# Performance work log

Hardware: AMD Instinct MI355X
Metric: run time of the kernel (lower is better)

The kernel has to match this reference:

```python
import jax, jax.numpy as jnp
import numpy as np

B, S = 1024, 512
V, E, H, T = 50000, 300, 800, 50


def setup_inputs() -> dict:
    key = jax.random.key(0)
    ks = jax.random.split(key, 8)
    ids = jax.random.randint(ks[0], (B, S), 0, V, dtype=jnp.int64 if jax.config.jax_enable_x64 else jnp.int32)
    return {
        "ids": ids,
        "rho": jax.random.normal(ks[1], (V, E), jnp.float32) * 0.02,
        "alpha": jax.random.normal(ks[2], (T, E), jnp.float32) * 0.02,
        "W1": jax.random.normal(ks[3], (E, H), jnp.float32) * 0.05,
        "b1": jnp.zeros((H,), jnp.float32),
        "Wmu": jax.random.normal(ks[4], (H, T), jnp.float32) * 0.05,
        "bmu": jnp.zeros((T,), jnp.float32),
        "Wlv": jax.random.normal(ks[5], (H, T), jnp.float32) * 0.05,
        "blv": jnp.zeros((T,), jnp.float32),
    }


def reference(ids, rho, alpha, W1, b1, Wmu, bmu, Wlv, blv):
    b, s = ids.shape
    v = rho.shape[0]
    # bag-of-words histogram: scatter-add instead of dense one_hot+reduce_sum
    bows = jnp.zeros((b, v), rho.dtype).at[jnp.arange(b)[:, None], ids].add(1.0)
    # zero out special tokens 1 and 2 (original: x * (1 - sum(one_hot([1,2]))))
    bows = bows.at[:, jnp.array([1, 2])].set(0.0)
    normal_bows = bows / jnp.sum(bows, axis=-1, keepdims=True)
    # encoder (eval mode: dropout is identity)
    x = jnp.einsum('bv,ve->be', normal_bows, rho)
    h = jax.nn.relu(x @ W1 + b1)
    mu_theta = h @ Wmu + bmu
    logsigma_theta = h @ Wlv + blv
    kl_theta = -0.5 * jnp.sum(1.0 + logsigma_theta - mu_theta**2 - jnp.exp(logsigma_theta), axis=-1)
    # reparameterize (eval/inference mode): z = mu
    theta = jax.nn.softmax(mu_theta, axis=-1)  # [B, T]
    beta = jax.nn.softmax(jnp.einsum('te,ve->tv', alpha, rho), axis=-1)  # [T, V]
    lookup = jnp.log(theta @ beta + 1e-5)  # [B, V]
    recon_loss = -jnp.sum(lookup * bows, axis=-1)
    loss = jnp.mean(recon_loss) + jnp.mean(kl_theta)
    return theta, loss
```

## Files before the change

kernel.cpp:

```cpp
#include <hip/hip_runtime.h>
#include <math.h>


#define Bn 1024
#define Sn 512
#define Vn 50000
#define En 300
#define Hn 800
#define Tn 50
#define KP 320
#define BSTR 64
#define W1FRAG_N (50 * 10 * 64 * 8)
#define WFRAG_N  (8 * 25 * 64 * 8)
#define NRANGE 8
#define VRANGE (Vn / NRANGE)

typedef __bf16 bf16x8 __attribute__((ext_vector_type(8)));
typedef float  f32x4  __attribute__((ext_vector_type(4)));

__device__ __forceinline__ float waveReduceSum(float v) {
    #pragma unroll
    for (int off = 32; off > 0; off >>= 1) v += __shfl_xor(v, off, 64);
    return v;
}
__device__ __forceinline__ float waveReduceMax(float v) {
    #pragma unroll
    for (int off = 32; off > 0; off >>= 1) v = fmaxf(v, __shfl_xor(v, off, 64));
    return v;
}
__device__ __forceinline__ unsigned short f2bf(float x) {
    unsigned u = __float_as_uint(x);
    return (unsigned short)((u + 0x7FFFu + ((u >> 16) & 1u)) >> 16);
}
__device__ __forceinline__ float bf_lo(unsigned u) { return __uint_as_float(u << 16); }
__device__ __forceinline__ float bf_hi(unsigned u) { return __uint_as_float(u & 0xFFFF0000u); }

__global__ __launch_bounds__(256) void k0_init(
        const float* __restrict__ alpha, unsigned short* __restrict__ bfrag,
        float* __restrict__ topicsum, float* __restrict__ loss,
        float* __restrict__ xbar) {
    const int gid = blockIdx.x * 256 + threadIdx.x;
    if (blockIdx.x == 0) {
        if (threadIdx.x < Tn) topicsum[threadIdx.x] = 0.f;
        if (threadIdx.x == 63) *loss = 0.f;
    }
    if (gid < Bn * En) xbar[gid] = 0.f;
    if (gid < 4 * 10 * 64 * 8) {
        int j = gid & 7;
        int lane = (gid >> 3) & 63;
        int rest = gid >> 9;
        int kt = rest % 10, w = rest / 10;
        int t = 16 * w + (lane & 15);
        int e = kt * 32 + (lane >> 4) * 8 + j;
        bfrag[gid] = (t < Tn && e < En) ? f2bf(alpha[t * En + e]) : (unsigned short)0;
    }
}

__global__ __launch_bounds__(256) void kp_prep(
        const float* __restrict__ W1, const float* __restrict__ Wmu,
        const float* __restrict__ Wlv, unsigned short* __restrict__ w1frag,
        unsigned short* __restrict__ wfrag) {
    const int gid = blockIdx.x * 256 + threadIdx.x;
    if (gid < W1FRAG_N) {
        int j = gid & 7, lane = (gid >> 3) & 63, rest = gid >> 9;
        int kt = rest % 10, nt = rest / 10;
        int e = kt * 32 + (lane >> 4) * 8 + j;
        int hcol = nt * 16 + (lane & 15);
        w1frag[gid] = (e < En) ? f2bf(W1[e * Hn + hcol]) : (unsigned short)0;
    } else {
        int g2 = gid - W1FRAG_N;
        if (g2 < WFRAG_N) {
            int j = g2 & 7, lane = (g2 >> 3) & 63, rest = g2 >> 9;
            int kt = rest % 25, nt = rest / 25;
            int k = kt * 32 + (lane >> 4) * 8 + j;
            int t = (nt & 3) * 16 + (lane & 15);
            float val = 0.f;
            if (t < Tn) val = (nt < 4) ? Wmu[k * Tn + t] : Wlv[k * Tn + t];
            wfrag[g2] = f2bf(val);
        }
    }
}

__global__ __launch_bounds__(256) void k5_cast(
        const float4* __restrict__ rho4, ushort4* __restrict__ rhoh4) {
    const int i = blockIdx.x * 256 + threadIdx.x;
    if (i < Vn * (KP / 4)) {
        int v = i / (KP / 4), s = i - v * (KP / 4);
        ushort4 p = {0, 0, 0, 0};
        if (s < En / 4) {
            float4 r = rho4[v * (En / 4) + s];
            p.x = f2bf(r.x); p.y = f2bf(r.y); p.z = f2bf(r.z); p.w = f2bf(r.w);
        }
        rhoh4[i] = p;
    }
}

__global__ __launch_bounds__(256) void k4_beta(
        const unsigned short* __restrict__ rhoh,
        const unsigned short* __restrict__ bfrag,
        unsigned int* __restrict__ betaU32, float* __restrict__ topicsum) {
    __shared__ unsigned short trans[64 * 66];
    const int tid = threadIdx.x;
    const int wave = tid >> 6, lane = tid & 63;
    const int quad = lane >> 4, l15 = lane & 15;
    const int v0 = blockIdx.x * 64;

    bf16x8 bf[10];
    #pragma unroll
    for (int kt = 0; kt < 10; ++kt)
        bf[kt] = *(const bf16x8*)(bfrag + ((wave * 10 + kt) * 64 + lane) * 8);

    float ts = 0.f;
    #pragma unroll
    for (int mt = 0; mt < 4; ++mt) {
        const int vbase = v0 + mt * 16;
        int vrow = vbase + l15; if (vrow >= Vn) vrow = Vn - 1;
        const unsigned short* arow = rhoh + (size_t)vrow * KP + quad * 8;
        f32x4 acc = {0.f, 0.f, 0.f, 0.f};
        #pragma unroll
        for (int kt = 0; kt < 10; ++kt) {
            bf16x8 a = *(const bf16x8*)(arow + kt * 32);
            acc = __builtin_amdgcn_mfma_f32_16x16x32_bf16(a, bf[kt], acc, 0, 0, 0);
        }
        #pragma unroll
        for (int r = 0; r < 4; ++r) {
            int vv = vbase + quad * 4 + r;
            float ev = (vv < Vn) ? expf(acc[r]) : 0.f;
            ts += ev;
            trans[(mt * 16 + quad * 4 + r) * 66 + 16 * wave + l15] = f2bf(ev);
        }
    }
    ts += __shfl_xor(ts, 16, 64);
    ts += __shfl_xor(ts, 32, 64);
    const int t = 16 * wave + l15;
    if (lane < 16 && t < Tn) atomicAdd(&topicsum[t], ts);
    __syncthreads();
    unsigned int* dst = betaU32 + (size_t)v0 * 32;
    const unsigned int* tr32 = (const unsigned int*)trans;
    for (int i = tid; i < 64 * 32; i += 256)
        dst[i] = tr32[(i >> 5) * 33 + (i & 31)];
}

__global__ __launch_bounds__(256) void k1_tokens_x(
        const int* __restrict__ ids, const unsigned int* __restrict__ rhoh32,
        int* __restrict__ toks, int* __restrict__ cnt,
        float* __restrict__ xbar) {
    __shared__ int sid[Sn];
    __shared__ int sfid[Sn];
    __shared__ int scount, sfull;
    const int blk = blockIdx.x;
    const int r = blk & (NRANGE - 1), b = blk >> 3;
    const int tid = threadIdx.x;
    const int lo = r * VRANGE, hi = lo + VRANGE;
    if (tid == 0) { scount = 0; sfull = 0; }
    __syncthreads();
    #pragma unroll
    for (int s0 = 0; s0 < Sn; s0 += 256) {
        int id = ids[b * Sn + s0 + tid];
        bool val = (id != 1 && id != 2);
        if (val && id >= lo && id < hi) {
            int p = atomicAdd(&scount, 1);
            sid[p] = id;
        }
        if (r == 0 && val) {
            int p = atomicAdd(&sfull, 1);
            sfid[p] = id;
        }
    }
    __syncthreads();
    if (r == 0) {
        const int nf = sfull;
        for (int i = tid; i < nf; i += 256) toks[b * Sn + i] = sfid[i];
        if (tid == 0) cnt[b] = nf;
    }
    const int m = scount;
    if (tid < En / 2) {
        float ax = 0.f, ay = 0.f;
        for (int s = 0; s < m; ++s) {
            unsigned u = rhoh32[sid[s] * (KP / 2) + tid];
            ax += bf_lo(u);
            ay += bf_hi(u);
        }
        if (m > 0) {
            atomicAdd(&xbar[b * En + 2 * tid], ax);
            atomicAdd(&xbar[b * En + 2 * tid + 1], ay);
        }
    }
}

__global__ __launch_bounds__(256) void k2a_xcast(
        const float* __restrict__ xbar, const int* __restrict__ cnt,
        unsigned short* __restrict__ xbh) {
    const int gid = blockIdx.x * 256 + threadIdx.x;
    if (gid < Bn * KP) {
        int b = gid / KP, e = gid - b * KP;
        unsigned short out = 0;
        if (e < En) {
            float invn = 1.0f / (float)cnt[b];
            out = f2bf(xbar[b * En + e] * invn);
        }
        xbh[gid] = out;
    }
}

__global__ __launch_bounds__(256) void k2_h(
        const unsigned short* __restrict__ xbh,
        const unsigned short* __restrict__ w1frag,
        const float* __restrict__ b1, unsigned short* __restrict__ hbh) {
    const int tid = threadIdx.x;
    const int wave = tid >> 6, lane = tid & 63;
    const int quad = lane >> 4, l15 = lane & 15;
    const int b0 = blockIdx.x * 16;
    const int nt = blockIdx.y * 4 + wave;
    if (nt >= 50) return;
    const unsigned short* arow = xbh + (size_t)(b0 + l15) * KP + quad * 8;
    f32x4 acc = {0.f, 0.f, 0.f, 0.f};
    #pragma unroll
    for (int kt = 0; kt < 10; ++kt) {
        bf16x8 a = *(const bf16x8*)(arow + kt * 32);
        bf16x8 bv = *(const bf16x8*)(w1frag + ((size_t)(nt * 10 + kt) * 64 + lane) * 8);
        acc = __builtin_amdgcn_mfma_f32_16x16x32_bf16(a, bv, acc, 0, 0, 0);
    }
    const int col = nt * 16 + l15;
    const float bias = b1[col];
    #pragma unroll
    for (int r = 0; r < 4; ++r) {
        int row = b0 + quad * 4 + r;
        hbh[(size_t)row * Hn + col] = f2bf(fmaxf(acc[r] + bias, 0.f));
    }
}

__global__ __launch_bounds__(256) void k3_theta(
        const unsigned short* __restrict__ hbh,
        const unsigned short* __restrict__ wfrag,
        const float* __restrict__ bmu, const float* __restrict__ blv,
        float* __restrict__ theta, float* __restrict__ loss) {
    __shared__ float mlds[16 * 65];
    __shared__ float llds[16 * 65];
    const int tid = threadIdx.x;
    const int wave = tid >> 6, lane = tid & 63;
    const int quad = lane >> 4, l15 = lane & 15;
    const int b0 = blockIdx.x * 16;
    const unsigned short* arow = hbh + (size_t)(b0 + l15) * Hn + quad * 8;
    f32x4 am = {0.f, 0.f, 0.f, 0.f}, al = {0.f, 0.f, 0.f, 0.f};
    #pragma unroll
    for (int kt = 0; kt < 25; ++kt) {
        bf16x8 a  = *(const bf16x8*)(arow + kt * 32);
        bf16x8 bm = *(const bf16x8*)(wfrag + ((size_t)(wave * 25 + kt) * 64 + lane) * 8);
        bf16x8 bl = *(const bf16x8*)(wfrag + ((size_t)((4 + wave) * 25 + kt) * 64 + lane) * 8);
        am = __builtin_amdgcn_mfma_f32_16x16x32_bf16(a, bm, am, 0, 0, 0);
        al = __builtin_amdgcn_mfma_f32_16x16x32_bf16(a, bl, al, 0, 0, 0);
    }
    const int t = wave * 16 + l15;
    const float bm_ = (t < Tn) ? bmu[t] : 0.f;
    const float bl_ = (t < Tn) ? blv[t] : 0.f;
    #pragma unroll
    for (int r = 0; r < 4; ++r) {
        int row = quad * 4 + r;
        mlds[row * 65 + t] = am[r] + bm_;
        llds[row * 65 + t] = al[r] + bl_;
    }
    __syncthreads();
    const int tt = (lane < Tn) ? lane : (Tn - 1);
    const bool act = (lane < Tn);
    float klacc = 0.f;
    #pragma unroll
    for (int k = 0; k < 4; ++k) {
        int row = wave * 4 + k;
        float mu = mlds[row * 65 + tt];
        float lv = llds[row * 65 + tt];
        float m = waveReduceMax(act ? mu : -1e30f);
        float ex = act ? expf(mu - m) : 0.f;
        float ssum = waveReduceSum(ex);
        if (act) theta[(b0 + row) * Tn + lane] = ex / ssum;
        klacc += waveReduceSum(act ? (1.f + lv - mu * mu - expf(lv)) : 0.f);
    }
    if (lane == 0) atomicAdd(loss, -0.5f * klacc * (1.0f / (float)Bn));
}

__global__ __launch_bounds__(256) void k6_recon(
        const int* __restrict__ toks, const int* __restrict__ cnt,
        const float* __restrict__ theta, const float* __restrict__ topicsum,
        const unsigned short* __restrict__ betaUh, float* __restrict__ loss) {
    __shared__ float sw[Tn];
    __shared__ float swred[4];
    const int b = blockIdx.x, tid = threadIdx.x;
    if (tid < Tn) sw[tid] = theta[b * Tn + tid] / topicsum[tid];
    __syncthreads();
    float wr[Tn];
    #pragma unroll
    for (int t = 0; t < Tn; ++t) wr[t] = sw[t];
    float lsum = 0.f;
    const int n = cnt[b];
    for (int i = tid; i < n; i += 256) {
        int v = toks[b * Sn + i];
        const uint4* q = (const uint4*)(betaUh + (size_t)v * BSTR);
        float dot = 0.f;
        #pragma unroll
        for (int k = 0; k < 6; ++k) {
            uint4 u = q[k];
            int t = 8 * k;
            dot += wr[t]     * bf_lo(u.x) + wr[t + 1] * bf_hi(u.x);
            dot += wr[t + 2] * bf_lo(u.y) + wr[t + 3] * bf_hi(u.y);
            dot += wr[t + 4] * bf_lo(u.z) + wr[t + 5] * bf_hi(u.z);
            dot += wr[t + 6] * bf_lo(u.w) + wr[t + 7] * bf_hi(u.w);
        }
        unsigned d = ((const unsigned*)q)[24];
        dot += wr[48] * bf_lo(d) + wr[49] * bf_hi(d);
        lsum += logf(dot + 1e-5f);
    }
    float s = waveReduceSum(lsum);
    const int wave = tid >> 6, lane = tid & 63;
    if (lane == 0) swred[wave] = s;
    __syncthreads();
    if (tid == 0) {
        float tot = swred[0] + swred[1] + swred[2] + swred[3];
        atomicAdd(loss, -tot * (1.0f / (float)Bn));
    }
}

extern "C" void kernel_launch(void* const* d_in, const int* in_sizes, int n_in,
                              void* d_out, int out_size, void* d_ws, size_t ws_size,
                              hipStream_t stream) {
    const int*   ids   = (const int*)d_in[0];
    const float* rho   = (const float*)d_in[1];
    const float* alpha = (const float*)d_in[2];
    const float* W1    = (const float*)d_in[3];
    const float* b1    = (const float*)d_in[4];
    const float* Wmu   = (const float*)d_in[5];
    const float* bmu   = (const float*)d_in[6];
    const float* Wlv   = (const float*)d_in[7];
    const float* blv   = (const float*)d_in[8];

    float* theta = (float*)d_out;
    float* loss  = theta + Bn * Tn;

    const int k4grid = (Vn + 63) / 64;
    char* w = (char*)d_ws;
    float* topicsum = (float*)w;                w += 256;
    unsigned short* bfrag = (unsigned short*)w; w += 4 * 10 * 64 * 8 * 2;
    unsigned short* w1frag = (unsigned short*)w; w += (size_t)W1FRAG_N * 2;
    unsigned short* wfrag = (unsigned short*)w;  w += (size_t)WFRAG_N * 2;
    int*   cnt      = (int*)w;                  w += Bn * 4;
    int*   toks     = (int*)w;                  w += Bn * Sn * 4;
    float* xbar     = (float*)w;                w += Bn * En * 4;
    unsigned short* xbh = (unsigned short*)w;   w += (size_t)Bn * KP * 2;
    unsigned short* hbh = (unsigned short*)w;   w += (size_t)Bn * Hn * 2;
    unsigned short* rhoh = (unsigned short*)w;  w += (size_t)Vn * KP * 2;
    unsigned int* betaU32 = (unsigned int*)w;   w += (size_t)k4grid * 64 * 128;

    k0_init<<<(Bn * En + 255) / 256, 256, 0, stream>>>(alpha, bfrag, topicsum, loss, xbar);
    kp_prep<<<(W1FRAG_N + WFRAG_N + 255) / 256, 256, 0, stream>>>(
        W1, Wmu, Wlv, w1frag, wfrag);
    k5_cast<<<(Vn * (KP / 4) + 255) / 256, 256, 0, stream>>>(
        (const float4*)rho, (ushort4*)rhoh);
    k4_beta<<<k4grid, 256, 0, stream>>>(rhoh, bfrag, betaU32, topicsum);
    k1_tokens_x<<<Bn * NRANGE, 256, 0, stream>>>(ids, (const unsigned int*)rhoh,
                                                 toks, cnt, xbar);
    k2a_xcast<<<(Bn * KP + 255) / 256, 256, 0, stream>>>(xbar, cnt, xbh);
    k2_h<<<dim3(64, 13), 256, 0, stream>>>(xbh, w1frag, b1, hbh);
    k3_theta<<<64, 256, 0, stream>>>(hbh, wfrag, bmu, blv, theta, loss);
    k6_recon<<<Bn, 256, 0, stream>>>(toks, cnt, theta, topicsum,
                                     (const unsigned short*)betaU32, loss);
}
```

Baseline: 224.3 us.

## Fuse rho bf16 cast into beta kernel and split recon by vocab range

Removes the separate rho cast kernel; the beta kernel now reads fp32 rho, converts it to bf16 in registers, feeds the MFMA and writes the bf16 copy for later use. The token compaction buffer is dropped. The recon kernel now rescans ids per block and splits each batch row across 16 vocabulary ranges to get more parallelism, and the x-gather kernel uses 16 ranges too. This trades an extra ids rescan and more atomics on the loss for fewer launches and less global traffic.

```diff
diff --git a/kernel.cpp b/kernel.cpp
--- a/kernel.cpp
+++ b/kernel.cpp
@@ -12,11 +12,12 @@
 #define BSTR 64
 #define W1FRAG_N (50 * 10 * 64 * 8)
 #define WFRAG_N  (8 * 25 * 64 * 8)
-#define NRANGE 8
+#define NRANGE 16
 #define VRANGE (Vn / NRANGE)
 
 typedef __bf16 bf16x8 __attribute__((ext_vector_type(8)));
 typedef float  f32x4  __attribute__((ext_vector_type(4)));
+typedef unsigned short us8 __attribute__((ext_vector_type(8)));
 
 __device__ __forceinline__ float waveReduceSum(float v) {
     #pragma unroll
@@ -81,24 +82,10 @@
     }
 }
 
-__global__ __launch_bounds__(256) void k5_cast(
-        const float4* __restrict__ rho4, ushort4* __restrict__ rhoh4) {
-    const int i = blockIdx.x * 256 + threadIdx.x;
-    if (i < Vn * (KP / 4)) {
-        int v = i / (KP / 4), s = i - v * (KP / 4);
-        ushort4 p = {0, 0, 0, 0};
-        if (s < En / 4) {
-            float4 r = rho4[v * (En / 4) + s];
-            p.x = f2bf(r.x); p.y = f2bf(r.y); p.z = f2bf(r.z); p.w = f2bf(r.w);
-        }
-        rhoh4[i] = p;
-    }
-}
-
 __global__ __launch_bounds__(256) void k4_beta(
-        const unsigned short* __restrict__ rhoh,
-        const unsigned short* __restrict__ bfrag,
-        unsigned int* __restrict__ betaU32, float* __restrict__ topicsum) {
+        const float* __restrict__ rho, const unsigned short* __restrict__ bfrag,
+        unsigned int* __restrict__ betaU32, unsigned short* __restrict__ rhoh,
+        float* __restrict__ topicsum) {
     __shared__ unsigned short trans[64 * 66];
     const int tid = threadIdx.x;
     const int wave = tid >> 6, lane = tid & 63;
@@ -115,11 +102,28 @@
     for (int mt = 0; mt < 4; ++mt) {
         const int vbase = v0 + mt * 16;
         int vrow = vbase + l15; if (vrow >= Vn) vrow = Vn - 1;
-        const unsigned short* arow = rhoh + (size_t)vrow * KP + quad * 8;
+        const float* arow = rho + (size_t)vrow * En;
+        unsigned short* hrow = rhoh + (size_t)vrow * KP;
         f32x4 acc = {0.f, 0.f, 0.f, 0.f};
         #pragma unroll
         for (int kt = 0; kt < 10; ++kt) {
-            bf16x8 a = *(const bf16x8*)(arow + kt * 32);
+            const int c0 = quad * 8 + kt * 32;
+            float f[8];
+            if (kt < 9) {
+                float4 p = *(const float4*)(arow + c0);
+                float4 q = *(const float4*)(arow + c0 + 4);
+                f[0] = p.x; f[1] = p.y; f[2] = p.z; f[3] = p.w;
+                f[4] = q.x; f[5] = q.y; f[6] = q.z; f[7] = q.w;
+            } else {
+                #pragma unroll
+                for (int i = 0; i < 8; ++i)
+                    f[i] = (c0 + i < En) ? arow[c0 + i] : 0.f;
+            }
+            us8 pk;
+            #pragma unroll
+            for (int i = 0; i < 8; ++i) pk[i] = f2bf(f[i]);
+            *(us8*)(hrow + c0) = pk;
+            bf16x8 a = __builtin_bit_cast(bf16x8, pk);
             acc = __builtin_amdgcn_mfma_f32_16x16x32_bf16(a, bf[kt], acc, 0, 0, 0);
         }
         #pragma unroll
@@ -143,13 +147,11 @@
 
 __global__ __launch_bounds__(256) void k1_tokens_x(
         const int* __restrict__ ids, const unsigned int* __restrict__ rhoh32,
-        int* __restrict__ toks, int* __restrict__ cnt,
-        float* __restrict__ xbar) {
+        int* __restrict__ cnt, float* __restrict__ xbar) {
     __shared__ int sid[Sn];
-    __shared__ int sfid[Sn];
     __shared__ int scount, sfull;
     const int blk = blockIdx.x;
-    const int r = blk & (NRANGE - 1), b = blk >> 3;
+    const int r = blk & (NRANGE - 1), b = blk >> 4;
     const int tid = threadIdx.x;
     const int lo = r * VRANGE, hi = lo + VRANGE;
     if (tid == 0) { scount = 0; sfull = 0; }
@@ -162,29 +164,20 @@
             int p = atomicAdd(&scount, 1);
             sid[p] = id;
         }
-        if (r == 0 && val) {
-            int p = atomicAdd(&sfull, 1);
-            sfid[p] = id;
-        }
-    }
-    __syncthreads();
-    if (r == 0) {
-        const int nf = sfull;
-        for (int i = tid; i < nf; i += 256) toks[b * Sn + i] = sfid[i];
-        if (tid == 0) cnt[b] = nf;
-    }
+        if (r == 0 && val) atomicAdd(&sfull, 1);
+    }
+    __syncthreads();
+    if (r == 0 && tid == 0) cnt[b] = sfull;
     const int m = scount;
-    if (tid < En / 2) {
+    if (tid < En / 2 && m > 0) {
         float ax = 0.f, ay = 0.f;
         for (int s = 0; s < m; ++s) {
             unsigned u = rhoh32[sid[s] * (KP / 2) + tid];
             ax += bf_lo(u);
             ay += bf_hi(u);
         }
-        if (m > 0) {
-            atomicAdd(&xbar[b * En + 2 * tid], ax);
-            atomicAdd(&xbar[b * En + 2 * tid + 1], ay);
-        }
+        atomicAdd(&xbar[b * En + 2 * tid], ax);
+        atomicAdd(&xbar[b * En + 2 * tid + 1], ay);
     }
 }
 
@@ -279,21 +272,36 @@
 }
 
 __global__ __launch_bounds__(256) void k6_recon(
-        const int* __restrict__ toks, const int* __restrict__ cnt,
-        const float* __restrict__ theta, const float* __restrict__ topicsum,
+        const int* __restrict__ ids, const float* __restrict__ theta,
+        const float* __restrict__ topicsum,
         const unsigned short* __restrict__ betaUh, float* __restrict__ loss) {
     __shared__ float sw[Tn];
+    __shared__ int sid[Sn];
+    __shared__ int scount;
     __shared__ float swred[4];
-    const int b = blockIdx.x, tid = threadIdx.x;
+    const int blk = blockIdx.x;
+    const int r = blk & (NRANGE - 1), b = blk >> 4;
+    const int tid = threadIdx.x;
+    const int lo = r * VRANGE, hi = lo + VRANGE;
     if (tid < Tn) sw[tid] = theta[b * Tn + tid] / topicsum[tid];
+    if (tid == 0) scount = 0;
+    __syncthreads();
+    #pragma unroll
+    for (int s0 = 0; s0 < Sn; s0 += 256) {
+        int id = ids[b * Sn + s0 + tid];
+        if (id != 1 && id != 2 && id >= lo && id < hi) {
+            int p = atomicAdd(&scount, 1);
+            sid[p] = id;
+        }
+    }
     __syncthreads();
     float wr[Tn];
     #pragma unroll
     for (int t = 0; t < Tn; ++t) wr[t] = sw[t];
     float lsum = 0.f;
-    const int n = cnt[b];
+    const int n = scount;
     for (int i = tid; i < n; i += 256) {
-        int v = toks[b * Sn + i];
+        int v = sid[i];
         const uint4* q = (const uint4*)(betaUh + (size_t)v * BSTR);
         float dot = 0.f;
         #pragma unroll
@@ -315,7 +323,7 @@
     __syncthreads();
     if (tid == 0) {
         float tot = swred[0] + swred[1] + swred[2] + swred[3];
-        atomicAdd(loss, -tot * (1.0f / (float)Bn));
+        if (tot != 0.f) atomicAdd(loss, -tot * (1.0f / (float)Bn));
     }
 }
 
@@ -342,7 +350,6 @@
     unsigned short* w1frag = (unsigned short*)w; w += (size_t)W1FRAG_N * 2;
     unsigned short* wfrag = (unsigned short*)w;  w += (size_t)WFRAG_N * 2;
     int*   cnt      = (int*)w;                  w += Bn * 4;
-    int*   toks     = (int*)w;                  w += Bn * Sn * 4;
     float* xbar     = (float*)w;                w += Bn * En * 4;
     unsigned short* xbh = (unsigned short*)w;   w += (size_t)Bn * KP * 2;
     unsigned short* hbh = (unsigned short*)w;   w += (size_t)Bn * Hn * 2;
@@ -352,14 +359,12 @@
     k0_init<<<(Bn * En + 255) / 256, 256, 0, stream>>>(alpha, bfrag, topicsum, loss, xbar);
     kp_prep<<<(W1FRAG_N + WFRAG_N + 255) / 256, 256, 0, stream>>>(
         W1, Wmu, Wlv, w1frag, wfrag);
-    k5_cast<<<(Vn * (KP / 4) + 255) / 256, 256, 0, stream>>>(
-        (const float4*)rho, (ushort4*)rhoh);
-    k4_beta<<<k4grid, 256, 0, stream>>>(rhoh, bfrag, betaU32, topicsum);
+    k4_beta<<<k4grid, 256, 0, stream>>>(rho, bfrag, betaU32, rhoh, topicsum);
     k1_tokens_x<<<Bn * NRANGE, 256, 0, stream>>>(ids, (const unsigned int*)rhoh,
-                                                 toks, cnt, xbar);
+                                                 cnt, xbar);
     k2a_xcast<<<(Bn * KP + 255) / 256, 256, 0, stream>>>(xbar, cnt, xbh);
     k2_h<<<dim3(64, 13), 256, 0, stream>>>(xbh, w1frag, b1, hbh);
     k3_theta<<<64, 256, 0, stream>>>(hbh, wfrag, bmu, blv, theta, loss);
-    k6_recon<<<Bn, 256, 0, stream>>>(toks, cnt, theta, topicsum,
-                                     (const unsigned short*)betaU32, loss);
-}
+    k6_recon<<<Bn * NRANGE, 256, 0, stream>>>(ids, theta, topicsum,
+                                              (const unsigned short*)betaU32, loss);
+}
```

Result: slower. 433.2 us (+93.1%).

## Shrink beta tiles to 16 rows, replicate topic sums, merge prep kernels

Applied to the files above, without the earlier changes.

k4_beta now handles 16 vocabulary rows per block instead of 64, so the grid grows from about 782 to 3125 blocks. B fragments are loaded inside the k-loop rather than kept in registers, which lowers register pressure. Topic-sum atomics go to 8 replicated slots, and k6 adds those slots back together, to reduce contention on 50 addresses. The kp_prep weight-fragment kernel is folded into k0_init to save one launch. In exchange, each block does more loads of alpha fragments per row computed, and the final transpose store is done in smaller chunks.

```diff
diff --git a/kernel.cpp b/kernel.cpp
--- a/kernel.cpp
+++ b/kernel.cpp
@@ -36,14 +36,14 @@
 __device__ __forceinline__ float bf_hi(unsigned u) { return __uint_as_float(u & 0xFFFF0000u); }
 
 __global__ __launch_bounds__(256) void k0_init(
-        const float* __restrict__ alpha, unsigned short* __restrict__ bfrag,
-        float* __restrict__ topicsum, float* __restrict__ loss,
-        float* __restrict__ xbar) {
+        const float* __restrict__ alpha, const float* __restrict__ W1,
+        const float* __restrict__ Wmu, const float* __restrict__ Wlv,
+        unsigned short* __restrict__ bfrag, unsigned short* __restrict__ w1frag,
+        unsigned short* __restrict__ wfrag, float* __restrict__ topicsumR,
+        float* __restrict__ loss, float* __restrict__ xbar) {
     const int gid = blockIdx.x * 256 + threadIdx.x;
-    if (blockIdx.x == 0) {
-        if (threadIdx.x < Tn) topicsum[threadIdx.x] = 0.f;
-        if (threadIdx.x == 63) *loss = 0.f;
-    }
+    if (gid < 512) topicsumR[gid] = 0.f;
+    if (gid == 520) *loss = 0.f;
     if (gid < Bn * En) xbar[gid] = 0.f;
     if (gid < 4 * 10 * 64 * 8) {
         int j = gid & 7;
@@ -54,13 +54,6 @@
         int e = kt * 32 + (lane >> 4) * 8 + j;
         bfrag[gid] = (t < Tn && e < En) ? f2bf(alpha[t * En + e]) : (unsigned short)0;
     }
-}
-
-__global__ __launch_bounds__(256) void kp_prep(
-        const float* __restrict__ W1, const float* __restrict__ Wmu,
-        const float* __restrict__ Wlv, unsigned short* __restrict__ w1frag,
-        unsigned short* __restrict__ wfrag) {
-    const int gid = blockIdx.x * 256 + threadIdx.x;
     if (gid < W1FRAG_N) {
         int j = gid & 7, lane = (gid >> 3) & 63, rest = gid >> 9;
         int kt = rest % 10, nt = rest / 10;
@@ -98,46 +91,37 @@
 __global__ __launch_bounds__(256) void k4_beta(
         const unsigned short* __restrict__ rhoh,
         const unsigned short* __restrict__ bfrag,
-        unsigned int* __restrict__ betaU32, float* __restrict__ topicsum) {
-    __shared__ unsigned short trans[64 * 66];
+        unsigned int* __restrict__ betaU32, float* __restrict__ topicsumR) {
+    __shared__ unsigned short trans[16 * 66];
     const int tid = threadIdx.x;
     const int wave = tid >> 6, lane = tid & 63;
     const int quad = lane >> 4, l15 = lane & 15;
-    const int v0 = blockIdx.x * 64;
-
-    bf16x8 bf[10];
-    #pragma unroll
-    for (int kt = 0; kt < 10; ++kt)
-        bf[kt] = *(const bf16x8*)(bfrag + ((wave * 10 + kt) * 64 + lane) * 8);
-
+    const int v0 = blockIdx.x * 16;
+
+    const unsigned short* arow = rhoh + (size_t)(v0 + l15) * KP + quad * 8;
+    f32x4 acc = {0.f, 0.f, 0.f, 0.f};
+    #pragma unroll
+    for (int kt = 0; kt < 10; ++kt) {
+        bf16x8 a = *(const bf16x8*)(arow + kt * 32);
+        bf16x8 bv = *(const bf16x8*)(bfrag + ((wave * 10 + kt) * 64 + lane) * 8);
+        acc = __builtin_amdgcn_mfma_f32_16x16x32_bf16(a, bv, acc, 0, 0, 0);
+    }
     float ts = 0.f;
     #pragma unroll
-    for (int mt = 0; mt < 4; ++mt) {
-        const int vbase = v0 + mt * 16;
-        int vrow = vbase + l15; if (vrow >= Vn) vrow = Vn - 1;
-        const unsigned short* arow = rhoh + (size_t)vrow * KP + quad * 8;
-        f32x4 acc = {0.f, 0.f, 0.f, 0.f};
-        #pragma unroll
-        for (int kt = 0; kt < 10; ++kt) {
-            bf16x8 a = *(const bf16x8*)(arow + kt * 32);
-            acc = __builtin_amdgcn_mfma_f32_16x16x32_bf16(a, bf[kt], acc, 0, 0, 0);
-        }
-        #pragma unroll
-        for (int r = 0; r < 4; ++r) {
-            int vv = vbase + quad * 4 + r;
-            float ev = (vv < Vn) ? expf(acc[r]) : 0.f;
-            ts += ev;
-            trans[(mt * 16 + quad * 4 + r) * 66 + 16 * wave + l15] = f2bf(ev);
-        }
+    for (int r = 0; r < 4; ++r) {
+        float ev = expf(acc[r]);
+        ts += ev;
+        trans[(quad * 4 + r) * 66 + 16 * wave + l15] = f2bf(ev);
     }
     ts += __shfl_xor(ts, 16, 64);
     ts += __shfl_xor(ts, 32, 64);
     const int t = 16 * wave + l15;
-    if (lane < 16 && t < Tn) atomicAdd(&topicsum[t], ts);
+    if (lane < 16 && t < Tn)
+        atomicAdd(&topicsumR[(blockIdx.x & 7) * 64 + t], ts);
     __syncthreads();
     unsigned int* dst = betaU32 + (size_t)v0 * 32;
     const unsigned int* tr32 = (const unsigned int*)trans;
-    for (int i = tid; i < 64 * 32; i += 256)
+    for (int i = tid; i < 16 * 32; i += 256)
         dst[i] = tr32[(i >> 5) * 33 + (i & 31)];
 }
 
@@ -174,17 +158,15 @@
         if (tid == 0) cnt[b] = nf;
     }
     const int m = scount;
-    if (tid < En / 2) {
+    if (tid < En / 2 && m > 0) {
         float ax = 0.f, ay = 0.f;
         for (int s = 0; s < m; ++s) {
             unsigned u = rhoh32[sid[s] * (KP / 2) + tid];
             ax += bf_lo(u);
             ay += bf_hi(u);
         }
-        if (m > 0) {
-            atomicAdd(&xbar[b * En + 2 * tid], ax);
-            atomicAdd(&xbar[b * En + 2 * tid + 1], ay);
-        }
+        atomicAdd(&xbar[b * En + 2 * tid], ax);
+        atomicAdd(&xbar[b * En + 2 * tid + 1], ay);
     }
 }
 
@@ -280,12 +262,17 @@
 
 __global__ __launch_bounds__(256) void k6_recon(
         const int* __restrict__ toks, const int* __restrict__ cnt,
-        const float* __restrict__ theta, const float* __restrict__ topicsum,
+        const float* __restrict__ theta, const float* __restrict__ topicsumR,
         const unsigned short* __restrict__ betaUh, float* __restrict__ loss) {
     __shared__ float sw[Tn];
     __shared__ float swred[4];
     const int b = blockIdx.x, tid = threadIdx.x;
-    if (tid < Tn) sw[tid] = theta[b * Tn + tid] / topicsum[tid];
+    if (tid < Tn) {
+        float z = 0.f;
+        #pragma unroll
+        for (int j = 0; j < 8; ++j) z += topicsumR[j * 64 + tid];
+        sw[tid] = theta[b * Tn + tid] / z;
+    }
     __syncthreads();
     float wr[Tn];
     #pragma unroll
@@ -335,9 +322,8 @@
     float* theta = (float*)d_out;
     float* loss  = theta + Bn * Tn;
 
-    const int k4grid = (Vn + 63) / 64;
     char* w = (char*)d_ws;
-    float* topicsum = (float*)w;                w += 256;
+    float* topicsumR = (float*)w;               w += 8 * 64 * 4;
     unsigned short* bfrag = (unsigned short*)w; w += 4 * 10 * 64 * 8 * 2;
     unsigned short* w1frag = (unsigned short*)w; w += (size_t)W1FRAG_N * 2;
     unsigned short* wfrag = (unsigned short*)w;  w += (size_t)WFRAG_N * 2;
@@ -347,19 +333,19 @@
     unsigned short* xbh = (unsigned short*)w;   w += (size_t)Bn * KP * 2;
     unsigned short* hbh = (unsigned short*)w;   w += (size_t)Bn * Hn * 2;
     unsigned short* rhoh = (unsigned short*)w;  w += (size_t)Vn * KP * 2;
-    unsigned int* betaU32 = (unsigned int*)w;   w += (size_t)k4grid * 64 * 128;
-
-    k0_init<<<(Bn * En + 255) / 256, 256, 0, stream>>>(alpha, bfrag, topicsum, loss, xbar);
-    kp_prep<<<(W1FRAG_N + WFRAG_N + 255) / 256, 256, 0, stream>>>(
-        W1, Wmu, Wlv, w1frag, wfrag);
+    unsigned int* betaU32 = (unsigned int*)w;   w += (size_t)Vn * 128;
+
+    const int k0grid = (W1FRAG_N + WFRAG_N + 255) / 256;
+    k0_init<<<k0grid, 256, 0, stream>>>(alpha, W1, Wmu, Wlv, bfrag, w1frag,
+                                        wfrag, topicsumR, loss, xbar);
     k5_cast<<<(Vn * (KP / 4) + 255) / 256, 256, 0, stream>>>(
         (const float4*)rho, (ushort4*)rhoh);
-    k4_beta<<<k4grid, 256, 0, stream>>>(rhoh, bfrag, betaU32, topicsum);
+    k4_beta<<<Vn / 16, 256, 0, stream>>>(rhoh, bfrag, betaU32, topicsumR);
     k1_tokens_x<<<Bn * NRANGE, 256, 0, stream>>>(ids, (const unsigned int*)rhoh,
                                                  toks, cnt, xbar);
     k2a_xcast<<<(Bn * KP + 255) / 256, 256, 0, stream>>>(xbar, cnt, xbh);
     k2_h<<<dim3(64, 13), 256, 0, stream>>>(xbh, w1frag, b1, hbh);
     k3_theta<<<64, 256, 0, stream>>>(hbh, wfrag, bmu, blv, theta, loss);
-    k6_recon<<<Bn, 256, 0, stream>>>(toks, cnt, theta, topicsum,
+    k6_recon<<<Bn, 256, 0, stream>>>(toks, cnt, theta, topicsumR,
                                      (const unsigned short*)betaU32, loss);
 }
```

New measurement: 216.3 us. 1.04x faster.
